# Kernel tuning notes

Hardware: AMD Instinct MI355X
Metric: run time of the kernel (lower is better)

## Reference

```python
import jax, jax.numpy as jnp
import numpy as np

N_NODES = 50000
N_EDGES = 800000
IN_CH = 64
HID = 128


def setup_inputs() -> dict:
    key = jax.random.key(0)
    ks = jax.random.split(key, 8)
    s = 0.05
    x = jax.random.normal(ks[0], (N_NODES, IN_CH), dtype=jnp.float32)
    edge_index = jax.random.randint(ks[1], (2, N_EDGES), 0, N_NODES, dtype=jnp.int64)
    return {
        "x": x,
        "edge_index": edge_index,
        "W1l": jax.random.normal(ks[2], (HID, IN_CH), dtype=jnp.float32) * s,
        "b1l": jnp.zeros((HID,), dtype=jnp.float32),
        "W1r": jax.random.normal(ks[3], (HID, IN_CH), dtype=jnp.float32) * s,
        "W2l": jax.random.normal(ks[4], (HID, HID), dtype=jnp.float32) * s,
        "b2l": jnp.zeros((HID,), dtype=jnp.float32),
        "W2r": jax.random.normal(ks[5], (HID, HID), dtype=jnp.float32) * s,
        "Wrec": jax.random.normal(ks[6], (IN_CH, HID), dtype=jnp.float32) * s,
        "brec": jnp.zeros((IN_CH,), dtype=jnp.float32),
    }


def _sage_conv(x, src, dst, Wl, bl, Wr, n_nodes):
    # mean aggregation of source features at destination nodes
    msg_sum = jax.ops.segment_sum(x[src], dst, num_segments=n_nodes)  # [N, d]
    deg = jax.ops.segment_sum(jnp.ones((src.shape[0],), x.dtype), dst,
                              num_segments=n_nodes)  # [N]
    mean = msg_sum / jnp.maximum(deg, 1.0)[:, None]
    # SAGEConv: lin_l(aggr) + lin_r(x_i); lin_l has bias, lin_r does not
    return mean @ Wl.T + bl + x @ Wr.T


def reference(x, edge_index, W1l, b1l, W1r, W2l, b2l, W2r, Wrec, brec):
    src, dst = edge_index[0], edge_index[1]
    n = x.shape[0]
    h = _sage_conv(x, src, dst, W1l, b1l, W1r, n)
    h = jax.nn.relu(h)  # activation between layers, none after last
    z = _sage_conv(h, src, dst, W2l, b2l, W2r, n)
    x_recon = z @ Wrec.T + brec
    return (z, x_recon)
```

## Files before the change

### kernel.cpp

```cpp
#include <hip/hip_runtime.h>

#define N_NODES 50000
#define N_EDGES 800000
#define IN_CH 64
#define HID 128
#define NB_SCAN ((N_NODES + 255) / 256)

typedef short short8 __attribute__((ext_vector_type(8)));
typedef float f32x4 __attribute__((ext_vector_type(4)));

static __device__ __forceinline__ unsigned short f2bf(float f) {
    unsigned u = __float_as_uint(f);
    u += 0x7FFF + ((u >> 16) & 1);
    return (unsigned short)(u >> 16);
}
static __device__ __forceinline__ float bflo(unsigned v) { return __uint_as_float(v << 16); }
static __device__ __forceinline__ float bfhi(unsigned v) { return __uint_as_float(v & 0xFFFF0000u); }


__global__ __launch_bounds__(256) void k_cvt(const float* __restrict__ src,
                                             unsigned short* __restrict__ dst, int n4) {
    int i = blockIdx.x * 256 + threadIdx.x;
    if (i < n4) {
        float4 v = ((const float4*)src)[i];
        unsigned lo = f2bf(v.x) | ((unsigned)f2bf(v.y) << 16);
        unsigned hi = f2bf(v.z) | ((unsigned)f2bf(v.w) << 16);
        ((uint2*)dst)[i] = make_uint2(lo, hi);
    }
}

__global__ __launch_bounds__(256) void k_cvt_w(const float* __restrict__ W1l, const float* __restrict__ W1r,
                                               const float* __restrict__ W2l, const float* __restrict__ W2r,
                                               const float* __restrict__ Wrec, unsigned short* __restrict__ dst) {
    int i = blockIdx.x * 256 + threadIdx.x;
    int e = i * 4;
    if (e >= 57344) return;
    const float* src; int off;
    if (e < 8192)       { src = W1l;  off = 0; }
    else if (e < 16384) { src = W1r;  off = 8192; }
    else if (e < 32768) { src = W2l;  off = 16384; }
    else if (e < 49152) { src = W2r;  off = 32768; }
    else                { src = Wrec; off = 49152; }
    float4 v = *(const float4*)(src + (e - off));
    unsigned lo = f2bf(v.x) | ((unsigned)f2bf(v.y) << 16);
    unsigned hi = f2bf(v.z) | ((unsigned)f2bf(v.w) << 16);
    *(uint2*)(dst + e) = make_uint2(lo, hi);
}


__global__ __launch_bounds__(256) void k_deg(const int* __restrict__ ei, int* __restrict__ deg) {
    int e = blockIdx.x * 256 + threadIdx.x;
    if (e < N_EDGES) {
        int d = ei[N_EDGES + e];
        if ((unsigned)d < N_NODES) atomicAdd(&deg[d], 1);
    }
}

__global__ __launch_bounds__(256) void k_scan1(const int* __restrict__ deg,
                                               int* __restrict__ excl,
                                               int* __restrict__ bsum) {
    int gid = blockIdx.x * 256 + threadIdx.x;
    int v = (gid < N_NODES) ? deg[gid] : 0;
    int lane = threadIdx.x & 63, wv = threadIdx.x >> 6;
    int s = v;
    #pragma unroll
    for (int d = 1; d < 64; d <<= 1) {
        int t = __shfl_up(s, d);
        if (lane >= d) s += t;
    }
    __shared__ int wsum[4];
    if (lane == 63) wsum[wv] = s;
    __syncthreads();
    int add = 0;
    #pragma unroll
    for (int w = 0; w < 4; w++) add += (w < wv) ? wsum[w] : 0;
    s += add;
    if (gid < N_NODES) excl[gid] = s - v;
    if (threadIdx.x == 255) bsum[blockIdx.x] = s;
}

__global__ __launch_bounds__(256) void k_scan2(const int* __restrict__ bsum,
                                               int* __restrict__ bpre,
                                               int* __restrict__ offs) {
    int tid = threadIdx.x;
    int v = (tid < NB_SCAN) ? bsum[tid] : 0;
    int lane = tid & 63, wv = tid >> 6;
    int s = v;
    #pragma unroll
    for (int d = 1; d < 64; d <<= 1) {
        int t = __shfl_up(s, d);
        if (lane >= d) s += t;
    }
    __shared__ int wsum[4];
    if (lane == 63) wsum[wv] = s;
    __syncthreads();
    int add = 0;
    #pragma unroll
    for (int w = 0; w < 4; w++) add += (w < wv) ? wsum[w] : 0;
    s += add;
    if (tid < NB_SCAN) bpre[tid] = s - v;
    if (tid == NB_SCAN - 1) offs[N_NODES] = s;
}

__global__ __launch_bounds__(256) void k_scan3(const int* __restrict__ excl,
                                               const int* __restrict__ bpre,
                                               int* __restrict__ offs) {
    int gid = blockIdx.x * 256 + threadIdx.x;
    if (gid < N_NODES) offs[gid] = excl[gid] + bpre[blockIdx.x];
}

__global__ __launch_bounds__(256) void k_fill(const int* __restrict__ ei, const int* __restrict__ offs,
                                              int* __restrict__ cursor, int* __restrict__ csr) {
    int e = blockIdx.x * 256 + threadIdx.x;
    if (e < N_EDGES) {
        int s = ei[e];
        int d = ei[N_EDGES + e];
        if ((unsigned)d < N_NODES && (unsigned)s < N_NODES) {
            int pos = atomicAdd(&cursor[d], 1);
            csr[offs[d] + pos] = s;
        }
    }
}

__global__ __launch_bounds__(256) void k_agg64b(const unsigned short* __restrict__ X,
                                                const int* __restrict__ csr,
                                                const int* __restrict__ offs,
                                                unsigned short* __restrict__ out) {
    int wid = (blockIdx.x * 256 + threadIdx.x) >> 6;
    int lane = threadIdx.x & 63;
    if (wid >= N_NODES) return;
    int beg = offs[wid], end = offs[wid + 1];
    int degn = end - beg;
    float inv = 1.0f / (float)(degn > 0 ? degn : 1);
    int half = lane >> 5, hl = lane & 31;
    float sx = 0.f, sy = 0.f;
    for (int e = beg + half; e < end; e += 2) {
        int idx = csr[e];
        unsigned v = *(const unsigned*)(X + (size_t)idx * 64 + hl * 2);
        sx += bflo(v); sy += bfhi(v);
    }
    sx += __shfl_xor(sx, 32);
    sy += __shfl_xor(sy, 32);
    if (half == 0) {
        unsigned o = f2bf(sx * inv) | ((unsigned)f2bf(sy * inv) << 16);
        *(unsigned*)(out + (size_t)wid * 64 + hl * 2) = o;
    }
}

__global__ __launch_bounds__(256) void k_agg128b(const unsigned short* __restrict__ X,
                                                 const int* __restrict__ csr,
                                                 const int* __restrict__ offs,
                                                 unsigned short* __restrict__ out) {
    int wid = (blockIdx.x * 256 + threadIdx.x) >> 6;
    int lane = threadIdx.x & 63;
    if (wid >= N_NODES) return;
    int beg = offs[wid], end = offs[wid + 1];
    int degn = end - beg;
    float inv = 1.0f / (float)(degn > 0 ? degn : 1);
    float sx = 0.f, sy = 0.f;
    int e = beg;
    for (; e + 2 <= end; e += 2) {
        int i0 = csr[e], i1 = csr[e + 1];
        unsigned a = *(const unsigned*)(X + (size_t)i0 * 128 + lane * 2);
        unsigned b = *(const unsigned*)(X + (size_t)i1 * 128 + lane * 2);
        sx += bflo(a) + bflo(b);
        sy += bfhi(a) + bfhi(b);
    }
    if (e < end) {
        unsigned a = *(const unsigned*)(X + (size_t)csr[e] * 128 + lane * 2);
        sx += bflo(a); sy += bfhi(a);
    }
    unsigned o = f2bf(sx * inv) | ((unsigned)f2bf(sy * inv) << 16);
    *(unsigned*)(out + (size_t)wid * 128 + lane * 2) = o;
}


template <int NOUT, int KTOT, bool DUAL, bool RELU, bool WF32, bool WBF16>
__global__ __launch_bounds__(256) void k_gemm_mfma(const unsigned short* __restrict__ A0,
                                                   const unsigned short* __restrict__ A1,
                                                   const unsigned short* __restrict__ W0,
                                                   const unsigned short* __restrict__ W1,
                                                   const float* __restrict__ bias,
                                                   float* __restrict__ out,
                                                   unsigned short* __restrict__ outb) {
    constexpr int K1 = DUAL ? KTOT / 2 : KTOT;
    constexpr int NF = NOUT / 16;
    int lane = threadIdx.x & 63;
    int wv = threadIdx.x >> 6;
    int m0 = blockIdx.x * 64 + wv * 16;
    int arow = m0 + (lane & 15);
    if (arow >= N_NODES) arow = N_NODES - 1;
    int kg = lane >> 4;

    f32x4 acc[NF] = {};

    #pragma unroll
    for (int ks = 0; ks < KTOT / 32; ks++) {
        int k0 = ks * 32;
        const unsigned short* Ap; const unsigned short* Wp; int kk;
        if (DUAL && k0 >= K1) { Ap = A1; Wp = W1; kk = k0 - K1; }
        else                  { Ap = A0; Wp = W0; kk = k0; }
        short8 a = *(const short8*)(Ap + (size_t)arow * K1 + kk + kg * 8);
        #pragma unroll
        for (int j = 0; j < NF; j++) {
            short8 b = *(const short8*)(Wp + (size_t)(j * 16 + (lane & 15)) * K1 + kk + kg * 8);
            acc[j] = __builtin_amdgcn_mfma_f32_16x16x32_bf16(a, b, acc[j], 0, 0, 0);
        }
    }

    int col = lane & 15;
    int r0 = (lane >> 4) * 4;
    #pragma unroll
    for (int j = 0; j < NF; j++) {
        float bv = bias[j * 16 + col];
        #pragma unroll
        for (int r = 0; r < 4; r++) {
            int grow = m0 + r0 + r;
            if (grow < N_NODES) {
                float v = acc[j][r] + bv;
                if (RELU) v = fmaxf(v, 0.f);
                if (WF32)  out[(size_t)grow * NOUT + j * 16 + col] = v;
                if (WBF16) outb[(size_t)grow * NOUT + j * 16 + col] = f2bf(v);
            }
        }
    }
}


extern "C" void kernel_launch(void* const* d_in, const int* in_sizes, int n_in,
                              void* d_out, int out_size, void* d_ws, size_t ws_size,
                              hipStream_t stream) {
    const float* x    = (const float*)d_in[0];
    const int*   ei   = (const int*)d_in[1];
    const float* W1l  = (const float*)d_in[2];
    const float* b1l  = (const float*)d_in[3];
    const float* W1r  = (const float*)d_in[4];
    const float* W2l  = (const float*)d_in[5];
    const float* b2l  = (const float*)d_in[6];
    const float* W2r  = (const float*)d_in[7];
    const float* Wrec = (const float*)d_in[8];
    const float* brec = (const float*)d_in[9];

    float* z    = (float*)d_out;
    float* xrec = (float*)d_out + (size_t)N_NODES * HID;

    char* ws = (char*)d_ws;
    int*   deg    = (int*)(ws);
    int*   offs   = (int*)(ws + (256u << 10));
    int*   cursor = (int*)(ws + (512u << 10));
    int*   excl   = (int*)(ws + (768u << 10));
    int*   bsum   = (int*)(ws + (1024u << 10));
    int*   bpre   = (int*)(ws + (1028u << 10));
    int*   csr    = (int*)(ws + (2u << 20));
    unsigned short* wb     = (unsigned short*)(ws + (5632u << 10));
    unsigned short* xb     = (unsigned short*)(ws + (7u  << 20));
    unsigned short* hb     = (unsigned short*)(ws + (14u << 20));
    unsigned short* mean1b = (unsigned short*)(ws + (27u << 20));
    unsigned short* mean2b = (unsigned short*)(ws + (27u << 20));
    unsigned short* zb     = (unsigned short*)(ws + (40u << 20));

    unsigned short* W1lb  = wb;
    unsigned short* W1rb  = wb + 8192;
    unsigned short* W2lb  = wb + 16384;
    unsigned short* W2rb  = wb + 32768;
    unsigned short* Wrecb = wb + 49152;

    hipMemsetAsync(deg, 0, N_NODES * sizeof(int), stream);
    hipMemsetAsync(cursor, 0, N_NODES * sizeof(int), stream);

    int egrid = (N_EDGES + 255) / 256;
    int ngrid = (N_NODES + 63) / 64;

    k_cvt_w<<<56, 256, 0, stream>>>(W1l, W1r, W2l, W2r, Wrec, wb);
    k_cvt<<<(800000 + 255) / 256, 256, 0, stream>>>(x, xb, 800000);

    k_deg<<<egrid, 256, 0, stream>>>(ei, deg);
    k_scan1<<<NB_SCAN, 256, 0, stream>>>(deg, excl, bsum);
    k_scan2<<<1, 256, 0, stream>>>(bsum, bpre, offs);
    k_scan3<<<NB_SCAN, 256, 0, stream>>>(excl, bpre, offs);
    k_fill<<<egrid, 256, 0, stream>>>(ei, offs, cursor, csr);

    k_agg64b<<<N_NODES / 4, 256, 0, stream>>>(xb, csr, offs, mean1b);
    k_gemm_mfma<128, 128, true, true, false, true>
        <<<ngrid, 256, 0, stream>>>(mean1b, xb, W1lb, W1rb, b1l, nullptr, hb);
    k_agg128b<<<N_NODES / 4, 256, 0, stream>>>(hb, csr, offs, mean2b);
    k_gemm_mfma<128, 256, true, false, true, true>
        <<<ngrid, 256, 0, stream>>>(mean2b, hb, W2lb, W2rb, b2l, z, zb);
    k_gemm_mfma<64, 128, false, false, true, false>
        <<<ngrid, 256, 0, stream>>>(zb, nullptr, Wrecb, nullptr, brec, xrec, nullptr);
}
```

Before: 349.6 us.

## Split gather aggregation into column slices and stage GEMM weights in LDS

Aggregation kernels now run once per 32-channel slice. Each wavefront handles four edges at a time over 16 lanes, and the CSR index is read with a nontemporal load. The intent is to shrink the working set of each gather pass so the random feature reads hit cache better. The GEMM now copies each weight matrix into XOR-swizzled shared memory before the MFMA loop instead of reloading it from global memory per wave. The cost is that the CSR is read several times over several launches, and the GEMM gains extra barriers and LDS use that may lower occupancy.

```diff
diff --git a/kernel.cpp b/kernel.cpp
--- a/kernel.cpp
+++ b/kernel.cpp
@@ -122,60 +122,36 @@
     }
 }
 
-__global__ __launch_bounds__(256) void k_agg64b(const unsigned short* __restrict__ X,
+
+template <int CH>
+__global__ __launch_bounds__(256) void k_agg_cs(const unsigned short* __restrict__ X,
                                                 const int* __restrict__ csr,
                                                 const int* __restrict__ offs,
-                                                unsigned short* __restrict__ out) {
+                                                unsigned short* __restrict__ out,
+                                                int c0) {
     int wid = (blockIdx.x * 256 + threadIdx.x) >> 6;
     int lane = threadIdx.x & 63;
     if (wid >= N_NODES) return;
     int beg = offs[wid], end = offs[wid + 1];
     int degn = end - beg;
     float inv = 1.0f / (float)(degn > 0 ? degn : 1);
-    int half = lane >> 5, hl = lane & 31;
+    int g = lane >> 4, hl = lane & 15;
     float sx = 0.f, sy = 0.f;
-    for (int e = beg + half; e < end; e += 2) {
-        int idx = csr[e];
-        unsigned v = *(const unsigned*)(X + (size_t)idx * 64 + hl * 2);
+    for (int e = beg + g; e < end; e += 4) {
+        int idx = __builtin_nontemporal_load(&csr[e]);
+        unsigned v = *(const unsigned*)(X + (size_t)idx * CH + c0 + hl * 2);
         sx += bflo(v); sy += bfhi(v);
     }
-    sx += __shfl_xor(sx, 32);
-    sy += __shfl_xor(sy, 32);
-    if (half == 0) {
+    sx += __shfl_xor(sx, 16); sy += __shfl_xor(sy, 16);
+    sx += __shfl_xor(sx, 32); sy += __shfl_xor(sy, 32);
+    if (g == 0) {
         unsigned o = f2bf(sx * inv) | ((unsigned)f2bf(sy * inv) << 16);
-        *(unsigned*)(out + (size_t)wid * 64 + hl * 2) = o;
-    }
-}
-
-__global__ __launch_bounds__(256) void k_agg128b(const unsigned short* __restrict__ X,
-                                                 const int* __restrict__ csr,
-                                                 const int* __restrict__ offs,
-                                                 unsigned short* __restrict__ out) {
-    int wid = (blockIdx.x * 256 + threadIdx.x) >> 6;
-    int lane = threadIdx.x & 63;
-    if (wid >= N_NODES) return;
-    int beg = offs[wid], end = offs[wid + 1];
-    int degn = end - beg;
-    float inv = 1.0f / (float)(degn > 0 ? degn : 1);
-    float sx = 0.f, sy = 0.f;
-    int e = beg;
-    for (; e + 2 <= end; e += 2) {
-        int i0 = csr[e], i1 = csr[e + 1];
-        unsigned a = *(const unsigned*)(X + (size_t)i0 * 128 + lane * 2);
-        unsigned b = *(const unsigned*)(X + (size_t)i1 * 128 + lane * 2);
-        sx += bflo(a) + bflo(b);
-        sy += bfhi(a) + bfhi(b);
-    }
-    if (e < end) {
-        unsigned a = *(const unsigned*)(X + (size_t)csr[e] * 128 + lane * 2);
-        sx += bflo(a); sy += bfhi(a);
-    }
-    unsigned o = f2bf(sx * inv) | ((unsigned)f2bf(sy * inv) << 16);
-    *(unsigned*)(out + (size_t)wid * 128 + lane * 2) = o;
-}
-
-
-template <int NOUT, int KTOT, bool DUAL, bool RELU, bool WF32, bool WBF16>
+        *(unsigned*)(out + (size_t)wid * CH + c0 + hl * 2) = o;
+    }
+}
+
+
+template <int NOUT, int K1, bool DUAL, bool RELU, bool WF32, bool WBF16>
 __global__ __launch_bounds__(256) void k_gemm_mfma(const unsigned short* __restrict__ A0,
                                                    const unsigned short* __restrict__ A1,
                                                    const unsigned short* __restrict__ W0,
@@ -183,28 +159,47 @@
                                                    const float* __restrict__ bias,
                                                    float* __restrict__ out,
                                                    unsigned short* __restrict__ outb) {
-    constexpr int K1 = DUAL ? KTOT / 2 : KTOT;
     constexpr int NF = NOUT / 16;
-    int lane = threadIdx.x & 63;
-    int wv = threadIdx.x >> 6;
+    constexpr int NPH = DUAL ? 2 : 1;
+    __shared__ char wlds[NOUT * K1 * 2];
+    int tid = threadIdx.x;
+    int lane = tid & 63;
+    int wv = tid >> 6;
     int m0 = blockIdx.x * 64 + wv * 16;
-    int arow = m0 + (lane & 15);
+    int col16 = lane & 15;
+    int kg = lane >> 4;
+    int arow = m0 + col16;
     if (arow >= N_NODES) arow = N_NODES - 1;
-    int kg = lane >> 4;
 
     f32x4 acc[NF] = {};
 
     #pragma unroll
-    for (int ks = 0; ks < KTOT / 32; ks++) {
-        int k0 = ks * 32;
-        const unsigned short* Ap; const unsigned short* Wp; int kk;
-        if (DUAL && k0 >= K1) { Ap = A1; Wp = W1; kk = k0 - K1; }
-        else                  { Ap = A0; Wp = W0; kk = k0; }
-        short8 a = *(const short8*)(Ap + (size_t)arow * K1 + kk + kg * 8);
+    for (int ph = 0; ph < NPH; ph++) {
+        const unsigned short* Wp = ph ? W1 : W0;
+        const unsigned short* Ap = ph ? A1 : A0;
+        if (ph) __syncthreads();
+        constexpr int CHUNKS = NOUT * K1 / 8;
         #pragma unroll
-        for (int j = 0; j < NF; j++) {
-            short8 b = *(const short8*)(Wp + (size_t)(j * 16 + (lane & 15)) * K1 + kk + kg * 8);
-            acc[j] = __builtin_amdgcn_mfma_f32_16x16x32_bf16(a, b, acc[j], 0, 0, 0);
+        for (int it = 0; it < CHUNKS / 256; it++) {
+            int ci = tid + it * 256;
+            int j = ci / (K1 / 8);
+            int c = (ci % (K1 / 8)) * 8;
+            short8 w = *(const short8*)(Wp + (size_t)j * K1 + c);
+            int byte = ((j * K1 + c) * 2) ^ ((j & 7) << 4);
+            *(short8*)(wlds + byte) = w;
+        }
+        __syncthreads();
+        #pragma unroll
+        for (int ks = 0; ks < K1 / 32; ks++) {
+            int kk = ks * 32;
+            short8 a = *(const short8*)(Ap + (size_t)arow * K1 + kk + kg * 8);
+            #pragma unroll
+            for (int j = 0; j < NF; j++) {
+                int row = j * 16 + col16;
+                int byte = ((row * K1 + kk + kg * 8) * 2) ^ ((row & 7) << 4);
+                short8 b = *(const short8*)(wlds + byte);
+                acc[j] = __builtin_amdgcn_mfma_f32_16x16x32_bf16(a, b, acc[j], 0, 0, 0);
+            }
         }
     }
 
@@ -253,11 +248,11 @@
     int*   bpre   = (int*)(ws + (1028u << 10));
     int*   csr    = (int*)(ws + (2u << 20));
     unsigned short* wb     = (unsigned short*)(ws + (5632u << 10));
-    unsigned short* xb     = (unsigned short*)(ws + (7u  << 20));
-    unsigned short* hb     = (unsigned short*)(ws + (14u << 20));
-    unsigned short* mean1b = (unsigned short*)(ws + (27u << 20));
-    unsigned short* mean2b = (unsigned short*)(ws + (27u << 20));
-    unsigned short* zb     = (unsigned short*)(ws + (40u << 20));
+    unsigned short* xb     = (unsigned short*)(ws + (6u  << 20));
+    unsigned short* mean1b = (unsigned short*)(ws + (13u << 20));
+    unsigned short* mean2b = (unsigned short*)(ws + (13u << 20));
+    unsigned short* hb     = (unsigned short*)(ws + (26u << 20));
+    unsigned short* zb     = (unsigned short*)(ws + (39u << 20));
 
     unsigned short* W1lb  = wb;
     unsigned short* W1rb  = wb + 8192;
@@ -265,11 +260,12 @@
     unsigned short* W2rb  = wb + 32768;
     unsigned short* Wrecb = wb + 49152;
 
-    hipMemsetAsync(deg, 0, N_NODES * sizeof(int), stream);
-    hipMemsetAsync(cursor, 0, N_NODES * sizeof(int), stream);
+    (void)hipMemsetAsync(deg, 0, N_NODES * sizeof(int), stream);
+    (void)hipMemsetAsync(cursor, 0, N_NODES * sizeof(int), stream);
 
     int egrid = (N_EDGES + 255) / 256;
     int ngrid = (N_NODES + 63) / 64;
+    int agrid = N_NODES / 4;
 
     k_cvt_w<<<56, 256, 0, stream>>>(W1l, W1r, W2l, W2r, Wrec, wb);
     k_cvt<<<(800000 + 255) / 256, 256, 0, stream>>>(x, xb, 800000);
@@ -280,11 +276,13 @@
     k_scan3<<<NB_SCAN, 256, 0, stream>>>(excl, bpre, offs);
     k_fill<<<egrid, 256, 0, stream>>>(ei, offs, cursor, csr);
 
-    k_agg64b<<<N_NODES / 4, 256, 0, stream>>>(xb, csr, offs, mean1b);
-    k_gemm_mfma<128, 128, true, true, false, true>
+    for (int c = 0; c < 64; c += 32)
+        k_agg_cs<64><<<agrid, 256, 0, stream>>>(xb, csr, offs, mean1b, c);
+    k_gemm_mfma<128, 64, true, true, false, true>
         <<<ngrid, 256, 0, stream>>>(mean1b, xb, W1lb, W1rb, b1l, nullptr, hb);
-    k_agg128b<<<N_NODES / 4, 256, 0, stream>>>(hb, csr, offs, mean2b);
-    k_gemm_mfma<128, 256, true, false, true, true>
+    for (int c = 0; c < 128; c += 32)
+        k_agg_cs<128><<<agrid, 256, 0, stream>>>(hb, csr, offs, mean2b, c);
+    k_gemm_mfma<128, 128, true, false, true, true>
         <<<ngrid, 256, 0, stream>>>(mean2b, hb, W2lb, W2rb, b2l, z, zb);
     k_gemm_mfma<64, 128, false, false, true, false>
         <<<ngrid, 256, 0, stream>>>(zb, nullptr, Wrecb, nullptr, brec, xrec, nullptr);
```

Result: slower. 406.7 us (+16.3%).
